# Optimization experiments

Measured on AMD Instinct MI355X. Metric: run time of the kernel, lower is better.

The kernel has to match this reference:

```python
import jax, jax.numpy as jnp
import numpy as np

SELF_OBS_DIM = 18
NBR_OBS_DIM = 6
NUM_NBR = 8
HID = 128

def _mlp2(x, W1, b1, W2, b2):
    return jnp.tanh(jnp.tanh(x @ W1 + b1) @ W2 + b2)

def setup_inputs() -> dict:
    key = jax.random.key(0)
    ks = jax.random.split(key, 20)
    B = 65536
    def w(k, i, o):
        return (jax.random.normal(k, (i, o), jnp.float32) / np.sqrt(i)).astype(jnp.float32)
    inp = {
        "self_obs": jax.random.normal(ks[0], (B, SELF_OBS_DIM), jnp.float32),
        "obs": jax.random.normal(ks[1], (B, SELF_OBS_DIM + NUM_NBR * NBR_OBS_DIM), jnp.float32),
        # embedding_mlp
        "e_W1": w(ks[2], SELF_OBS_DIM + NBR_OBS_DIM, HID), "e_b1": jnp.zeros((HID,), jnp.float32),
        "e_W2": w(ks[3], HID, HID), "e_b2": jnp.zeros((HID,), jnp.float32),
        # neighbor_value_mlp
        "v_W1": w(ks[4], HID, HID), "v_b1": jnp.zeros((HID,), jnp.float32),
        "v_W2": w(ks[5], HID, HID), "v_b2": jnp.zeros((HID,), jnp.float32),
        # attention_mlp
        "a_W1": w(ks[6], 2 * HID, HID), "a_b1": jnp.zeros((HID,), jnp.float32),
        "a_W2": w(ks[7], HID, HID), "a_b2": jnp.zeros((HID,), jnp.float32),
        "a_W3": w(ks[8], HID, 1), "a_b3": jnp.zeros((1,), jnp.float32),
        "all_neighbor_obs_size": NUM_NBR * NBR_OBS_DIM,
        "batch_size": B,
    }
    return inp

def reference(self_obs, obs, e_W1, e_b1, e_W2, e_b2, v_W1, v_b1, v_W2, v_b2,
              a_W1, a_b1, a_W2, a_b2, a_W3, a_b3, all_neighbor_obs_size, batch_size):
    B = batch_size
    n = NUM_NBR
    # slice out neighbor obs; reshape is batch-major: row index = b*n + k
    obs_nb = obs[:, SELF_OBS_DIM:SELF_OBS_DIM + all_neighbor_obs_size].reshape(-1, NBR_OBS_DIM)
    # torch .repeat(n, 1) tiles whole batch -> neighbor-major: row index = k*B + b (kept faithful)
    self_rep = jnp.tile(self_obs, (n, 1))
    emb = _mlp2(jnp.concatenate([self_rep, obs_nb], axis=1), e_W1, e_b1, e_W2, e_b2)  # [B*n, H]
    vals = _mlp2(emb, v_W1, v_b1, v_W2, v_b2)                                          # [B*n, H]
    emb_mean = emb.reshape(B, n, HID).mean(axis=1)                                     # [B, H]
    mean_rep = jnp.tile(emb_mean, (n, 1))                                              # [B*n, H]
    h = jnp.tanh(jnp.concatenate([emb, mean_rep], axis=1) @ a_W1 + a_b1)
    h = jnp.tanh(h @ a_W2 + a_b2)
    scores = (h @ a_W3 + a_b3).reshape(B, n)
    attn = jax.nn.softmax(scores, axis=1).reshape(-1, 1)
    out = (attn * vals).reshape(B, n, HID).sum(axis=1)                                 # [B, H]
    return out
```

## Files before the change

kernel.cpp:

```cpp
#include <hip/hip_runtime.h>
#include <math.h>

#define BATCH 65536
#define HID   128
#define NTHREADS 256

using bf16x8 = __attribute__((ext_vector_type(8))) short;
using f32x4  = __attribute__((ext_vector_type(4))) float;

#define E1H 0
#define E1L 4096
#define SWB 8192
#define BIASF 204800
#define MEANH 206592
#define WS_ELEMS_FULL (MEANH + BATCH*HID)

__device__ __forceinline__ float4 ld4(const float* p) { return *reinterpret_cast<const float4*>(p); }

__device__ __forceinline__ unsigned cvtpk(float a, float b) {
    unsigned r;
    asm("v_cvt_pk_bf16_f32 %0, %1, %2" : "=v"(r) : "v"(a), "v"(b));
    return r;
}

__device__ __forceinline__ float tanh_f(float x) {
    float t = __builtin_amdgcn_exp2f(x * 2.8853900817779268f);
    float r = __builtin_amdgcn_rcpf(t + 1.f);
    return 1.f - 2.f * r;
}

__device__ __forceinline__ f32x4 mfma16(bf16x8 a, bf16x8 b, f32x4 c) {
    return __builtin_amdgcn_mfma_f32_16x16x32_bf16(a, b, c, 0, 0, 0);
}

__device__ __forceinline__ bf16x8 pk8(unsigned u0, unsigned u1, unsigned u2, unsigned u3) {
    union { unsigned u[4]; bf16x8 v; } x;
    x.u[0] = u0; x.u[1] = u1; x.u[2] = u2; x.u[3] = u3;
    return x.v;
}

__device__ __forceinline__ void split_pack(float v0, float v1, float v2, float v3,
        unsigned& uh0, unsigned& uh1, unsigned& ul0, unsigned& ul1) {
    uh0 = cvtpk(v0, v1); uh1 = cvtpk(v2, v3);
    float f0 = __uint_as_float(uh0 << 16), f1 = __uint_as_float(uh0 & 0xffff0000u);
    float f2 = __uint_as_float(uh1 << 16), f3 = __uint_as_float(uh1 & 0xffff0000u);
    ul0 = cvtpk(v0 - f0, v1 - f1); ul1 = cvtpk(v2 - f2, v3 - f3);
}

__device__ __forceinline__ void zacc(f32x4 acc[2][8]) {
    #pragma unroll
    for (int rt = 0; rt < 2; ++rt)
        #pragma unroll
        for (int t = 0; t < 8; ++t) acc[rt][t] = f32x4{0.f, 0.f, 0.f, 0.f};
}

__device__ __forceinline__ int permc(int p) {
    return 32 * ((p >> 4) & 3) + 8 * ((p >> 2) & 3) + 4 * (p >> 6) + (p & 3);
}

__device__ __forceinline__ void gload16(const void* g, void* l) {
    __builtin_amdgcn_global_load_lds(
        (const __attribute__((address_space(1))) void*)g,
        (__attribute__((address_space(3))) void*)l, 16, 0, 0);
}
__device__ __forceinline__ void stage64k(short* dst, const short* __restrict__ src,
                                         int w, int lane) {
    const char* g = (const char*)src + w * 16384 + lane * 16;
    char* l = (char*)dst + w * 16384;
    #pragma unroll
    for (int s = 0; s < 16; ++s) gload16(g + s * 1024, l + s * 1024);
}

template<int TERMS>
__device__ __forceinline__ void mm_lds(f32x4 acc[2][8],
        const bf16x8 Bh[2][4], const bf16x8 Bl[2][4],
        const short* Wlds, int sE, int sO)
{
    #pragma unroll
    for (int tp = 0; tp < 4; ++tp) {
        #pragma unroll
        for (int ks = 0; ks < 4; ++ks) {
            const int base = ((ks & 1) ? sO : sE) + (ks >> 1) * 64 + tp * 4096;
            bf16x8 wh0 = *(const bf16x8*)(Wlds + base);
            bf16x8 wh1 = *(const bf16x8*)(Wlds + base + 2048);
            bf16x8 wl0 = *(const bf16x8*)(Wlds + base + 16384);
            bf16x8 wl1 = *(const bf16x8*)(Wlds + base + 16384 + 2048);
            __builtin_amdgcn_s_setprio(1);
            acc[0][2*tp  ] = mfma16(wh0, Bh[0][ks], acc[0][2*tp  ]);
            acc[0][2*tp+1] = mfma16(wh1, Bh[0][ks], acc[0][2*tp+1]);
            acc[1][2*tp  ] = mfma16(wh0, Bh[1][ks], acc[1][2*tp  ]);
            acc[1][2*tp+1] = mfma16(wh1, Bh[1][ks], acc[1][2*tp+1]);
            acc[0][2*tp  ] = mfma16(wl0, Bh[0][ks], acc[0][2*tp  ]);
            acc[0][2*tp+1] = mfma16(wl1, Bh[0][ks], acc[0][2*tp+1]);
            acc[1][2*tp  ] = mfma16(wl0, Bh[1][ks], acc[1][2*tp  ]);
            acc[1][2*tp+1] = mfma16(wl1, Bh[1][ks], acc[1][2*tp+1]);
            if constexpr (TERMS == 3) {
                acc[0][2*tp  ] = mfma16(wh0, Bl[0][ks], acc[0][2*tp  ]);
                acc[0][2*tp+1] = mfma16(wh1, Bl[0][ks], acc[0][2*tp+1]);
                acc[1][2*tp  ] = mfma16(wh0, Bl[1][ks], acc[1][2*tp  ]);
                acc[1][2*tp+1] = mfma16(wh1, Bl[1][ks], acc[1][2*tp+1]);
            }
            __builtin_amdgcn_s_setprio(0);
        }
    }
}

__device__ __forceinline__ void mm_l1(f32x4 acc[2][8],
        const bf16x8 X0h[2], const bf16x8 X0l[2],
        const short* __restrict__ Wh, const short* __restrict__ Wl, int wb)
{
    #pragma unroll
    for (int tp = 0; tp < 4; ++tp) {
        const short* whp = Wh + wb + tp * 1024;
        const short* wlp = Wl + wb + tp * 1024;
        bf16x8 wh0 = *(const bf16x8*)(whp);
        bf16x8 wh1 = *(const bf16x8*)(whp + 512);
        bf16x8 wl0 = *(const bf16x8*)(wlp);
        bf16x8 wl1 = *(const bf16x8*)(wlp + 512);
        __builtin_amdgcn_s_setprio(1);
        acc[0][2*tp  ] = mfma16(wh0, X0h[0], acc[0][2*tp  ]);
        acc[0][2*tp+1] = mfma16(wh1, X0h[0], acc[0][2*tp+1]);
        acc[1][2*tp  ] = mfma16(wh0, X0h[1], acc[1][2*tp  ]);
        acc[1][2*tp+1] = mfma16(wh1, X0h[1], acc[1][2*tp+1]);
        acc[0][2*tp  ] = mfma16(wh0, X0l[0], acc[0][2*tp  ]);
        acc[0][2*tp+1] = mfma16(wh1, X0l[0], acc[0][2*tp+1]);
        acc[1][2*tp  ] = mfma16(wh0, X0l[1], acc[1][2*tp  ]);
        acc[1][2*tp+1] = mfma16(wh1, X0l[1], acc[1][2*tp+1]);
        acc[0][2*tp  ] = mfma16(wl0, X0h[0], acc[0][2*tp  ]);
        acc[0][2*tp+1] = mfma16(wl1, X0h[0], acc[0][2*tp+1]);
        acc[1][2*tp  ] = mfma16(wl0, X0h[1], acc[1][2*tp  ]);
        acc[1][2*tp+1] = mfma16(wl1, X0h[1], acc[1][2*tp+1]);
        __builtin_amdgcn_s_setprio(0);
    }
}

__device__ __forceinline__ void epi_state(const f32x4 acc[2][8], const float* __restrict__ bp,
        int q4, bf16x8 Nh[2][4], bf16x8 Nl[2][4])
{
    #pragma unroll
    for (int ks = 0; ks < 4; ++ks) {
        float4 b0 = ld4(bp + 16 * ks + q4);
        float4 b1 = ld4(bp + 16 * ks + 64 + q4);
        #pragma unroll
        for (int rt = 0; rt < 2; ++rt) {
            unsigned h0, h1, h2, h3, l0, l1, l2, l3;
            split_pack(tanh_f(acc[rt][ks][0] + b0.x), tanh_f(acc[rt][ks][1] + b0.y),
                       tanh_f(acc[rt][ks][2] + b0.z), tanh_f(acc[rt][ks][3] + b0.w),
                       h0, h1, l0, l1);
            split_pack(tanh_f(acc[rt][ks+4][0] + b1.x), tanh_f(acc[rt][ks+4][1] + b1.y),
                       tanh_f(acc[rt][ks+4][2] + b1.z), tanh_f(acc[rt][ks+4][3] + b1.w),
                       h2, h3, l2, l3);
            Nh[rt][ks] = pk8(h0, h1, h2, h3);
            Nl[rt][ks] = pk8(l0, l1, l2, l3);
        }
    }
}

__device__ __forceinline__ void epi_state_hi(const f32x4 acc[2][8], const float* __restrict__ bp,
        int q4, bf16x8 Nh[2][4])
{
    #pragma unroll
    for (int ks = 0; ks < 4; ++ks) {
        float4 b0 = ld4(bp + 16 * ks + q4);
        float4 b1 = ld4(bp + 16 * ks + 64 + q4);
        #pragma unroll
        for (int rt = 0; rt < 2; ++rt) {
            unsigned h0 = cvtpk(tanh_f(acc[rt][ks][0] + b0.x), tanh_f(acc[rt][ks][1] + b0.y));
            unsigned h1 = cvtpk(tanh_f(acc[rt][ks][2] + b0.z), tanh_f(acc[rt][ks][3] + b0.w));
            unsigned h2 = cvtpk(tanh_f(acc[rt][ks+4][0] + b1.x), tanh_f(acc[rt][ks+4][1] + b1.y));
            unsigned h3 = cvtpk(tanh_f(acc[rt][ks+4][2] + b1.z), tanh_f(acc[rt][ks+4][3] + b1.w));
            Nh[rt][ks] = pk8(h0, h1, h2, h3);
        }
    }
}

__device__ __forceinline__ void build_x0(bf16x8 X0h[2], bf16x8 X0l[2],
        const float* __restrict__ self_obs, const float* __restrict__ obs,
        int r0w, int lm, int q)
{
    #pragma unroll
    for (int rt = 0; rt < 2; ++rt) {
        int row = r0w + 16 * rt + lm;
        const float* sp = self_obs + (size_t)(row & (BATCH - 1)) * 18;
        float x0 = 0.f, x1 = 0.f, x2 = 0.f, x3 = 0.f, x4 = 0.f, x5 = 0.f, x6 = 0.f, x7 = 0.f;
        if (q == 0) {
            x0 = sp[0]; x1 = sp[1]; x2 = sp[2]; x3 = sp[3];
            x4 = sp[4]; x5 = sp[5]; x6 = sp[6]; x7 = sp[7];
        } else if (q == 1) {
            x0 = sp[8]; x1 = sp[9]; x2 = sp[10]; x3 = sp[11];
            x4 = sp[12]; x5 = sp[13]; x6 = sp[14]; x7 = sp[15];
        } else if (q == 2) {
            x0 = sp[16]; x1 = sp[17];
            const float* op = obs + (size_t)(row >> 3) * 66 + 18 + (row & 7) * 6;
            x2 = op[0]; x3 = op[1]; x4 = op[2]; x5 = op[3]; x6 = op[4]; x7 = op[5];
        }
        unsigned h0, h1, h2, h3, l0, l1, l2, l3;
        split_pack(x0, x1, x2, x3, h0, h1, l0, l1);
        split_pack(x4, x5, x6, x7, h2, h3, l2, l3);
        X0h[rt] = pk8(h0, h1, h2, h3);
        X0l[rt] = pk8(l0, l1, l2, l3);
    }
}

__device__ __forceinline__ int remap(int hw) {
    return (((hw >> 3) & 7) << 9) | ((hw & 7) << 6) | (hw >> 6);
}

__global__ void prep_w(const float* __restrict__ eW1, const float* __restrict__ eW2,
                       const float* __restrict__ vW1, const float* __restrict__ vW2,
                       const float* __restrict__ aW1, const float* __restrict__ aW2,
                       const float* __restrict__ eb1, const float* __restrict__ eb2,
                       const float* __restrict__ vb1, const float* __restrict__ vb2,
                       const float* __restrict__ ab1, const float* __restrict__ ab2,
                       const float* __restrict__ aW3,
                       short* __restrict__ ws)
{
    int t = blockIdx.x * blockDim.x + threadIdx.x;
    if (t >= 103296) return;
    if (t >= 102400) {
        int i = t - 102400, arr = i >> 7, p = i & 127;
        int c = permc(p);
        float v;
        if      (arr == 0) v = eb1[c];
        else if (arr == 1) v = eb2[c];
        else if (arr == 2) v = vb1[c];
        else if (arr == 3) v = vb2[c];
        else if (arr == 4) v = ab1[c];
        else if (arr == 5) v = ab2[c];
        else               v = aW3[c];
        ((float*)(ws + BIASF))[arr * 128 + p] = v;
        return;
    }
    float v; int dh, dl;
    if (t < 4096) {
        int p = t >> 5, k = t & 31;
        v = (k < 24) ? eW1[k * HID + permc(p)] : 0.f;
        dh = E1H + t; dl = E1L + t;
    } else {
        int u = t - 4096;
        int blob = u >> 14, vv = u & 16383;
        int p = vv >> 7;
        int k = (vv & 127) ^ ((p & 7) << 3);
        int c = permc(p);
        if      (blob == 0) v = eW2[k * HID + c];
        else if (blob == 1) v = aW1[k * HID + c];
        else if (blob == 2) v = aW1[(128 + k) * HID + c];
        else if (blob == 3) v = aW2[k * HID + c];
        else if (blob == 4) v = vW1[k * HID + c];
        else                v = vW2[k * HID + c];
        dh = SWB + blob * 32768 + vv;
        dl = dh + 16384;
    }
    unsigned uu = __float_as_uint(v);
    unsigned h = (uu + 0x7fffu + ((uu >> 16) & 1u)) >> 16;
    float lf = v - __uint_as_float(h << 16);
    ws[dh] = (short)h;
    ws[dl] = (short)(__float_as_uint(lf) >> 16);
}

__global__ __launch_bounds__(NTHREADS, 2)
void qk_mean(const float* __restrict__ self_obs, const float* __restrict__ obs,
             short* ws)
{
    __shared__ __align__(16) short Wb[32768];
    const int tid = threadIdx.x, lane = tid & 63, w = tid >> 6;
    const int lm = lane & 15, q = lane >> 4;
    const int r0w = remap(blockIdx.x) * 128 + w * 32;
    const float* bf = (const float*)(ws + BIASF);
    const int sE = (lm * 128 + 8 * q) ^ ((lm & 7) << 3);
    const int sO = (lm * 128 + 8 * q + 32) ^ ((lm & 7) << 3);

    stage64k(Wb, ws + SWB, w, lane);

    f32x4 acc[2][8];
    bf16x8 X0h[2], X0l[2];
    build_x0(X0h, X0l, self_obs, obs, r0w, lm, q);
    zacc(acc);
    mm_l1(acc, X0h, X0l, ws + E1H, ws + E1L, lm * 32 + q * 8);
    bf16x8 Hh[2][4], Hl[2][4];
    epi_state(acc, bf, q * 4, Hh, Hl);
    __syncthreads();

    zacc(acc);
    mm_lds<3>(acc, Hh, Hl, Wb, sE, sO);

    const float* b2 = bf + 128;
    short* mh = ws + MEANH;
    #pragma unroll
    for (int rt = 0; rt < 2; ++rt) {
        float m[8][4];
        #pragma unroll
        for (int ks = 0; ks < 4; ++ks) {
            float4 b0 = ld4(b2 + 16 * ks + 4 * q);
            float4 b1 = ld4(b2 + 16 * ks + 64 + 4 * q);
            m[ks][0] = tanh_f(acc[rt][ks][0] + b0.x);
            m[ks][1] = tanh_f(acc[rt][ks][1] + b0.y);
            m[ks][2] = tanh_f(acc[rt][ks][2] + b0.z);
            m[ks][3] = tanh_f(acc[rt][ks][3] + b0.w);
            m[ks+4][0] = tanh_f(acc[rt][ks+4][0] + b1.x);
            m[ks+4][1] = tanh_f(acc[rt][ks+4][1] + b1.y);
            m[ks+4][2] = tanh_f(acc[rt][ks+4][2] + b1.z);
            m[ks+4][3] = tanh_f(acc[rt][ks+4][3] + b1.w);
        }
        #pragma unroll
        for (int t = 0; t < 8; ++t)
            #pragma unroll
            for (int e = 0; e < 4; ++e) {
                float v = m[t][e];
                v += __shfl_xor(v, 1); v += __shfl_xor(v, 2); v += __shfl_xor(v, 4);
                m[t][e] = v * 0.125f;
            }
        if ((lm & 7) == 0) {
            int g = (r0w >> 3) + 2 * rt + (lm >> 3);
            #pragma unroll
            for (int ks = 0; ks < 4; ++ks) {
                unsigned h0 = cvtpk(m[ks][0], m[ks][1]);
                unsigned h1 = cvtpk(m[ks][2], m[ks][3]);
                unsigned h2 = cvtpk(m[ks+4][0], m[ks+4][1]);
                unsigned h3 = cvtpk(m[ks+4][2], m[ks+4][3]);
                *(bf16x8*)(mh + (size_t)g * 128 + 32 * ks + 8 * q) = pk8(h0, h1, h2, h3);
            }
        }
    }
}

__global__ __launch_bounds__(NTHREADS, 2)
void qk_main(const float* __restrict__ self_obs, const float* __restrict__ obs,
             short* ws, float* __restrict__ out)
{
    __shared__ __align__(16) short Wb[32768];
    const int tid = threadIdx.x, lane = tid & 63, w = tid >> 6;
    const int lm = lane & 15, q = lane >> 4;
    const int r0w = remap(blockIdx.x) * 128 + w * 32;
    const float* bf = (const float*)(ws + BIASF);
    const int sE = (lm * 128 + 8 * q) ^ ((lm & 7) << 3);
    const int sO = (lm * 128 + 8 * q + 32) ^ ((lm & 7) << 3);

    f32x4 acc[2][8];
    float a0, a1;

    stage64k(Wb, ws + SWB + 0 * 32768, w, lane);
    {
        bf16x8 X0h[2], X0l[2];
        build_x0(X0h, X0l, self_obs, obs, r0w, lm, q);
        zacc(acc);
        mm_l1(acc, X0h, X0l, ws + E1H, ws + E1L, lm * 32 + q * 8);
    }
    bf16x8 Hh[2][4], Hl[2][4];
    epi_state(acc, bf, q * 4, Hh, Hl);
    __syncthreads();

    zacc(acc);
    mm_lds<3>(acc, Hh, Hl, Wb, sE, sO);
    __syncthreads();
    stage64k(Wb, ws + SWB + 1 * 32768, w, lane);
    bf16x8 Mh[2][4];
    {
        const short* mh = ws + MEANH;
        const size_t mr0 = (size_t)((r0w + lm) & (BATCH - 1)) * 128;
        const size_t mr1 = (size_t)((r0w + 16 + lm) & (BATCH - 1)) * 128;
        #pragma unroll
        for (int ks = 0; ks < 4; ++ks) {
            Mh[0][ks] = *(const bf16x8*)(mh + mr0 + 32 * ks + 8 * q);
            Mh[1][ks] = *(const bf16x8*)(mh + mr1 + 32 * ks + 8 * q);
        }
    }
    bf16x8 Eh[2][4], El[2][4];
    epi_state(acc, bf + 128, q * 4, Eh, El);
    __syncthreads();

    zacc(acc);
    mm_lds<3>(acc, Eh, El, Wb, sE, sO);
    __syncthreads();
    stage64k(Wb, ws + SWB + 2 * 32768, w, lane);
    __syncthreads();

    mm_lds<2>(acc, Mh, Mh, Wb, sE, sO);
    __syncthreads();
    stage64k(Wb, ws + SWB + 3 * 32768, w, lane);
    bf16x8 Ah[2][4];
    epi_state_hi(acc, bf + 4 * 128, q * 4, Ah);
    __syncthreads();

    zacc(acc);
    mm_lds<2>(acc, Ah, Ah, Wb, sE, sO);
    __syncthreads();
    stage64k(Wb, ws + SWB + 4 * 32768, w, lane);
    {
        const float* b6  = bf + 5 * 128;
        const float* w3p = bf + 6 * 128;
        float p0 = 0.f, p1 = 0.f;
        #pragma unroll
        for (int t = 0; t < 8; ++t) {
            float4 b  = ld4(b6 + 16 * t + 4 * q);
            float4 wv = ld4(w3p + 16 * t + 4 * q);
            p0 += tanh_f(acc[0][t][0] + b.x) * wv.x + tanh_f(acc[0][t][1] + b.y) * wv.y
                + tanh_f(acc[0][t][2] + b.z) * wv.z + tanh_f(acc[0][t][3] + b.w) * wv.w;
            p1 += tanh_f(acc[1][t][0] + b.x) * wv.x + tanh_f(acc[1][t][1] + b.y) * wv.y
                + tanh_f(acc[1][t][2] + b.z) * wv.z + tanh_f(acc[1][t][3] + b.w) * wv.w;
        }
        p0 += __shfl_xor(p0, 16); p0 += __shfl_xor(p0, 32);
        p1 += __shfl_xor(p1, 16); p1 += __shfl_xor(p1, 32);
        float m0 = p0, m1 = p1;
        m0 = fmaxf(m0, __shfl_xor(m0, 1)); m0 = fmaxf(m0, __shfl_xor(m0, 2)); m0 = fmaxf(m0, __shfl_xor(m0, 4));
        m1 = fmaxf(m1, __shfl_xor(m1, 1)); m1 = fmaxf(m1, __shfl_xor(m1, 2)); m1 = fmaxf(m1, __shfl_xor(m1, 4));
        float e0 = __expf(p0 - m0), e1 = __expf(p1 - m1);
        float s0 = e0, s1 = e1;
        s0 += __shfl_xor(s0, 1); s0 += __shfl_xor(s0, 2); s0 += __shfl_xor(s0, 4);
        s1 += __shfl_xor(s1, 1); s1 += __shfl_xor(s1, 2); s1 += __shfl_xor(s1, 4);
        a0 = e0 * __builtin_amdgcn_rcpf(s0);
        a1 = e1 * __builtin_amdgcn_rcpf(s1);
    }
    __syncthreads();

    zacc(acc);
    mm_lds<3>(acc, Eh, El, Wb, sE, sO);
    __syncthreads();
    stage64k(Wb, ws + SWB + 5 * 32768, w, lane);
    bf16x8 Vh[2][4], Vl[2][4];
    epi_state(acc, bf + 2 * 128, q * 4, Vh, Vl);
    __syncthreads();

    zacc(acc);
    mm_lds<3>(acc, Vh, Vl, Wb, sE, sO);
    const float* b4 = bf + 3 * 128;
    #pragma unroll
    for (int rt = 0; rt < 2; ++rt) {
        const float av = rt ? a1 : a0;
        float o[8][4];
        #pragma unroll
        for (int ks = 0; ks < 4; ++ks) {
            float4 b0 = ld4(b4 + 16 * ks + 4 * q);
            float4 b1 = ld4(b4 + 16 * ks + 64 + 4 * q);
            o[ks][0] = av * tanh_f(acc[rt][ks][0] + b0.x);
            o[ks][1] = av * tanh_f(acc[rt][ks][1] + b0.y);
            o[ks][2] = av * tanh_f(acc[rt][ks][2] + b0.z);
            o[ks][3] = av * tanh_f(acc[rt][ks][3] + b0.w);
            o[ks+4][0] = av * tanh_f(acc[rt][ks+4][0] + b1.x);
            o[ks+4][1] = av * tanh_f(acc[rt][ks+4][1] + b1.y);
            o[ks+4][2] = av * tanh_f(acc[rt][ks+4][2] + b1.z);
            o[ks+4][3] = av * tanh_f(acc[rt][ks+4][3] + b1.w);
        }
        #pragma unroll
        for (int t = 0; t < 8; ++t)
            #pragma unroll
            for (int e = 0; e < 4; ++e) {
                float v = o[t][e];
                v += __shfl_xor(v, 1); v += __shfl_xor(v, 2); v += __shfl_xor(v, 4);
                o[t][e] = v;
            }
        if ((lm & 7) == 0) {
            int g = (r0w >> 3) + 2 * rt + (lm >> 3);
            #pragma unroll
            for (int ks = 0; ks < 4; ++ks) {
                *(float4*)(out + (size_t)g * 128 + 32 * ks + 8 * q) =
                    make_float4(o[ks][0], o[ks][1], o[ks][2], o[ks][3]);
                *(float4*)(out + (size_t)g * 128 + 32 * ks + 8 * q + 4) =
                    make_float4(o[ks+4][0], o[ks+4][1], o[ks+4][2], o[ks+4][3]);
            }
        }
    }
}

extern "C" void kernel_launch(void* const* d_in, const int* in_sizes, int n_in,
                              void* d_out, int out_size, void* d_ws, size_t ws_size,
                              hipStream_t stream) {
    const float* self_obs = (const float*)d_in[0];
    const float* obs      = (const float*)d_in[1];
    const float* eW1 = (const float*)d_in[2];  const float* eb1 = (const float*)d_in[3];
    const float* eW2 = (const float*)d_in[4];  const float* eb2 = (const float*)d_in[5];
    const float* vW1 = (const float*)d_in[6];  const float* vb1 = (const float*)d_in[7];
    const float* vW2 = (const float*)d_in[8];  const float* vb2 = (const float*)d_in[9];
    const float* aW1 = (const float*)d_in[10]; const float* ab1 = (const float*)d_in[11];
    const float* aW2 = (const float*)d_in[12]; const float* ab2 = (const float*)d_in[13];
    const float* aW3 = (const float*)d_in[14];
    float* out = (float*)d_out;
    short* ws = (short*)d_ws;

    prep_w<<<404, 256, 0, stream>>>(eW1, eW2, vW1, vW2, aW1, aW2,
                                    eb1, eb2, vb1, vb2, ab1, ab2, aW3, ws);

    dim3 grid(4096);
    qk_mean<<<grid, NTHREADS, 0, stream>>>(self_obs, obs, ws);
    qk_main<<<grid, NTHREADS, 0, stream>>>(self_obs, obs, ws, out);
}
```

Before: 385.9 us.

## Double-buffer weight quarters in LDS to cut footprint and raise occupancy

Replaces the 64KB single LDS weight buffer with two 16KB buffers, staging each layer's weights in quarters (hi/lo halves, two column halves) and overlapping the next quarter's async global-to-LDS load with MFMAs on the current one. Each layer prefetches the first quarter of the next layer. The smaller LDS footprint allows launch bounds of 4 blocks per CU instead of 2. The cost is more barriers per layer and tighter register limits at higher occupancy, which may cause spills.

```diff
diff --git a/kernel.cpp b/kernel.cpp
--- a/kernel.cpp
+++ b/kernel.cpp
@@ -63,46 +63,59 @@
         (const __attribute__((address_space(1))) void*)g,
         (__attribute__((address_space(3))) void*)l, 16, 0, 0);
 }
-__device__ __forceinline__ void stage64k(short* dst, const short* __restrict__ src,
-                                         int w, int lane) {
-    const char* g = (const char*)src + w * 16384 + lane * 16;
-    char* l = (char*)dst + w * 16384;
-    #pragma unroll
-    for (int s = 0; s < 16; ++s) gload16(g + s * 1024, l + s * 1024);
-}
-
-template<int TERMS>
-__device__ __forceinline__ void mm_lds(f32x4 acc[2][8],
+__device__ __forceinline__ void stage16k(short* dst, const short* __restrict__ src, int tid) {
+    const char* g = (const char*)src + tid * 16;
+    char* l = (char*)dst + tid * 16;
+    #pragma unroll
+    for (int s = 0; s < 4; ++s) gload16(g + s * 4096, l + s * 4096);
+}
+
+template<int NMUL, int TPH>
+__device__ __forceinline__ void mm_q(f32x4 acc[2][8],
         const bf16x8 Bh[2][4], const bf16x8 Bl[2][4],
-        const short* Wlds, int sE, int sO)
-{
-    #pragma unroll
-    for (int tp = 0; tp < 4; ++tp) {
+        const short* Wq, int sE, int sO)
+{
+    #pragma unroll
+    for (int tp = 0; tp < 2; ++tp) {
+        const int t0 = 4 * TPH + 2 * tp, t1 = t0 + 1;
         #pragma unroll
         for (int ks = 0; ks < 4; ++ks) {
             const int base = ((ks & 1) ? sO : sE) + (ks >> 1) * 64 + tp * 4096;
-            bf16x8 wh0 = *(const bf16x8*)(Wlds + base);
-            bf16x8 wh1 = *(const bf16x8*)(Wlds + base + 2048);
-            bf16x8 wl0 = *(const bf16x8*)(Wlds + base + 16384);
-            bf16x8 wl1 = *(const bf16x8*)(Wlds + base + 16384 + 2048);
+            bf16x8 w0 = *(const bf16x8*)(Wq + base);
+            bf16x8 w1 = *(const bf16x8*)(Wq + base + 2048);
             __builtin_amdgcn_s_setprio(1);
-            acc[0][2*tp  ] = mfma16(wh0, Bh[0][ks], acc[0][2*tp  ]);
-            acc[0][2*tp+1] = mfma16(wh1, Bh[0][ks], acc[0][2*tp+1]);
-            acc[1][2*tp  ] = mfma16(wh0, Bh[1][ks], acc[1][2*tp  ]);
-            acc[1][2*tp+1] = mfma16(wh1, Bh[1][ks], acc[1][2*tp+1]);
-            acc[0][2*tp  ] = mfma16(wl0, Bh[0][ks], acc[0][2*tp  ]);
-            acc[0][2*tp+1] = mfma16(wl1, Bh[0][ks], acc[0][2*tp+1]);
-            acc[1][2*tp  ] = mfma16(wl0, Bh[1][ks], acc[1][2*tp  ]);
-            acc[1][2*tp+1] = mfma16(wl1, Bh[1][ks], acc[1][2*tp+1]);
-            if constexpr (TERMS == 3) {
-                acc[0][2*tp  ] = mfma16(wh0, Bl[0][ks], acc[0][2*tp  ]);
-                acc[0][2*tp+1] = mfma16(wh1, Bl[0][ks], acc[0][2*tp+1]);
-                acc[1][2*tp  ] = mfma16(wh0, Bl[1][ks], acc[1][2*tp  ]);
-                acc[1][2*tp+1] = mfma16(wh1, Bl[1][ks], acc[1][2*tp+1]);
+            acc[0][t0] = mfma16(w0, Bh[0][ks], acc[0][t0]);
+            acc[0][t1] = mfma16(w1, Bh[0][ks], acc[0][t1]);
+            acc[1][t0] = mfma16(w0, Bh[1][ks], acc[1][t0]);
+            acc[1][t1] = mfma16(w1, Bh[1][ks], acc[1][t1]);
+            if (NMUL == 2) {
+                acc[0][t0] = mfma16(w0, Bl[0][ks], acc[0][t0]);
+                acc[0][t1] = mfma16(w1, Bl[0][ks], acc[0][t1]);
+                acc[1][t0] = mfma16(w0, Bl[1][ks], acc[1][t0]);
+                acc[1][t1] = mfma16(w1, Bl[1][ks], acc[1][t1]);
             }
             __builtin_amdgcn_s_setprio(0);
         }
     }
+}
+
+template<int NH>
+__device__ __forceinline__ void layer4(f32x4 acc[2][8],
+        const bf16x8 Bh[2][4], const bf16x8 Bl[2][4],
+        short* B0, short* B1, const short* __restrict__ src,
+        const short* __restrict__ next, int sE, int sO, int tid)
+{
+    stage16k(B1, src + 8192, tid);
+    mm_q<NH, 0>(acc, Bh, Bl, B0, sE, sO);
+    __syncthreads();
+    stage16k(B0, src + 16384, tid);
+    mm_q<NH, 1>(acc, Bh, Bl, B1, sE, sO);
+    __syncthreads();
+    stage16k(B1, src + 24576, tid);
+    mm_q<1, 0>(acc, Bh, Bh, B0, sE, sO);
+    __syncthreads();
+    if (next) stage16k(B0, next, tid);
+    mm_q<1, 1>(acc, Bh, Bh, B1, sE, sO);
 }
 
 __device__ __forceinline__ void mm_l1(f32x4 acc[2][8],
@@ -258,19 +271,19 @@
     ws[dl] = (short)(__float_as_uint(lf) >> 16);
 }
 
-__global__ __launch_bounds__(NTHREADS, 2)
+__global__ __launch_bounds__(NTHREADS, 4)
 void qk_mean(const float* __restrict__ self_obs, const float* __restrict__ obs,
              short* ws)
 {
-    __shared__ __align__(16) short Wb[32768];
-    const int tid = threadIdx.x, lane = tid & 63, w = tid >> 6;
+    __shared__ __align__(16) short B0[8192], B1[8192];
+    const int tid = threadIdx.x, lane = tid & 63;
     const int lm = lane & 15, q = lane >> 4;
-    const int r0w = remap(blockIdx.x) * 128 + w * 32;
+    const int r0w = remap(blockIdx.x) * 128 + (tid >> 6) * 32;
     const float* bf = (const float*)(ws + BIASF);
     const int sE = (lm * 128 + 8 * q) ^ ((lm & 7) << 3);
     const int sO = (lm * 128 + 8 * q + 32) ^ ((lm & 7) << 3);
 
-    stage64k(Wb, ws + SWB, w, lane);
+    stage16k(B0, ws + SWB, tid);
 
     f32x4 acc[2][8];
     bf16x8 X0h[2], X0l[2];
@@ -282,7 +295,7 @@
     __syncthreads();
 
     zacc(acc);
-    mm_lds<3>(acc, Hh, Hl, Wb, sE, sO);
+    layer4<2>(acc, Hh, Hl, B0, B1, ws + SWB, nullptr, sE, sO, tid);
 
     const float* b2 = bf + 128;
     short* mh = ws + MEANH;
@@ -324,14 +337,14 @@
     }
 }
 
-__global__ __launch_bounds__(NTHREADS, 2)
+__global__ __launch_bounds__(NTHREADS, 4)
 void qk_main(const float* __restrict__ self_obs, const float* __restrict__ obs,
              short* ws, float* __restrict__ out)
 {
-    __shared__ __align__(16) short Wb[32768];
-    const int tid = threadIdx.x, lane = tid & 63, w = tid >> 6;
+    __shared__ __align__(16) short B0[8192], B1[8192];
+    const int tid = threadIdx.x, lane = tid & 63;
     const int lm = lane & 15, q = lane >> 4;
-    const int r0w = remap(blockIdx.x) * 128 + w * 32;
+    const int r0w = remap(blockIdx.x) * 128 + (tid >> 6) * 32;
     const float* bf = (const float*)(ws + BIASF);
     const int sE = (lm * 128 + 8 * q) ^ ((lm & 7) << 3);
     const int sO = (lm * 128 + 8 * q + 32) ^ ((lm & 7) << 3);
@@ -339,7 +352,7 @@
     f32x4 acc[2][8];
     float a0, a1;
 
-    stage64k(Wb, ws + SWB + 0 * 32768, w, lane);
+    stage16k(B0, ws + SWB, tid);
     {
         bf16x8 X0h[2], X0l[2];
         build_x0(X0h, X0l, self_obs, obs, r0w, lm, q);
@@ -350,10 +363,6 @@
     epi_state(acc, bf, q * 4, Hh, Hl);
     __syncthreads();
 
-    zacc(acc);
-    mm_lds<3>(acc, Hh, Hl, Wb, sE, sO);
-    __syncthreads();
-    stage64k(Wb, ws + SWB + 1 * 32768, w, lane);
     bf16x8 Mh[2][4];
     {
         const short* mh = ws + MEANH;
@@ -365,27 +374,24 @@
             Mh[1][ks] = *(const bf16x8*)(mh + mr1 + 32 * ks + 8 * q);
         }
     }
+
+    zacc(acc);
+    layer4<2>(acc, Hh, Hl, B0, B1, ws + SWB, ws + SWB + 32768, sE, sO, tid);
     bf16x8 Eh[2][4], El[2][4];
     epi_state(acc, bf + 128, q * 4, Eh, El);
     __syncthreads();
 
     zacc(acc);
-    mm_lds<3>(acc, Eh, El, Wb, sE, sO);
-    __syncthreads();
-    stage64k(Wb, ws + SWB + 2 * 32768, w, lane);
-    __syncthreads();
-
-    mm_lds<2>(acc, Mh, Mh, Wb, sE, sO);
-    __syncthreads();
-    stage64k(Wb, ws + SWB + 3 * 32768, w, lane);
+    layer4<2>(acc, Eh, El, B0, B1, ws + SWB + 32768, ws + SWB + 2 * 32768, sE, sO, tid);
+    __syncthreads();
+
+    layer4<1>(acc, Mh, Mh, B0, B1, ws + SWB + 2 * 32768, ws + SWB + 3 * 32768, sE, sO, tid);
     bf16x8 Ah[2][4];
     epi_state_hi(acc, bf + 4 * 128, q * 4, Ah);
     __syncthreads();
 
     zacc(acc);
-    mm_lds<2>(acc, Ah, Ah, Wb, sE, sO);
-    __syncthreads();
-    stage64k(Wb, ws + SWB + 4 * 32768, w, lane);
+    layer4<1>(acc, Ah, Ah, B0, B1, ws + SWB + 3 * 32768, ws + SWB + 4 * 32768, sE, sO, tid);
     {
         const float* b6  = bf + 5 * 128;
         const float* w3p = bf + 6 * 128;
@@ -414,15 +420,13 @@
     __syncthreads();
 
     zacc(acc);
-    mm_lds<3>(acc, Eh, El, Wb, sE, sO);
-    __syncthreads();
-    stage64k(Wb, ws + SWB + 5 * 32768, w, lane);
+    layer4<2>(acc, Eh, El, B0, B1, ws + SWB + 4 * 32768, ws + SWB + 5 * 32768, sE, sO, tid);
     bf16x8 Vh[2][4], Vl[2][4];
     epi_state(acc, bf + 2 * 128, q * 4, Vh, Vl);
     __syncthreads();
 
     zacc(acc);
-    mm_lds<3>(acc, Vh, Vl, Wb, sE, sO);
+    layer4<2>(acc, Vh, Vl, B0, B1, ws + SWB + 5 * 32768, nullptr, sE, sO, tid);
     const float* b4 = bf + 3 * 128;
     #pragma unroll
     for (int rt = 0; rt < 2; ++rt) {
```

Result: slower. 539.1 us (+39.7%).
